# Performance work log

Measured on AMD Instinct MI355X. Metric: run time of the kernel, lower is better.

The kernel has to match this reference:

```python
import jax, jax.numpy as jnp
import numpy as np
from jax import lax

K = 5
WIN = (1, 1, K, K)
PAD = ((0, 0), (0, 0), (K // 2, K // 2), (K // 2, K // 2))
T_POOL = 0.9


def _conv(x, w, b, pad, dil=(1, 1), groups=1):
    y = lax.conv_general_dilated(x, w, (1, 1), pad, rhs_dilation=dil,
                                 dimension_numbers=('NCHW', 'OIHW', 'NCHW'),
                                 feature_group_count=groups)
    return y + b[None, :, None, None]


def _cbs(x, w, b):
    # Ultralytics Conv: 1x1 conv + folded-BN bias + SiLU
    return jax.nn.silu(_conv(x, w, b, ((0, 0), (0, 0))))


def _maxpool(x):
    return lax.reduce_window(x, -jnp.inf, lax.max, WIN, (1, 1, 1, 1), PAD)


def _sumpool(x):
    return lax.reduce_window(x, 0.0, lax.add, WIN, (1, 1, 1, 1), PAD)


def _tmaxavg(x):
    # TMaxAvgPool2d: blend of max pool and avg pool with weight T
    return T_POOL * _maxpool(x) + (1.0 - T_POOL) * (_sumpool(x) / (K * K))


def _rwpool(x):
    # RWPool2d: exponentially (response-) weighted pooling over the window
    c = lax.stop_gradient(jnp.max(x))  # constant shift, cancels exactly
    e = jnp.exp(x - c)
    return _sumpool(e * x) / (_sumpool(e) + 1e-6)


def setup_inputs():
    key = jax.random.key(0)
    ks = jax.random.split(key, 16)
    B, C1, H, W = 8, 512, 64, 64
    c_ = C1 // 2   # 256
    c4 = c_ * 4    # 1024
    C2 = 512
    f32 = jnp.float32

    def w(k, shape):
        return jax.random.normal(k, shape, f32) * 0.02

    return {
        'x': jax.random.normal(ks[0], (B, C1, H, W), f32),
        'w_sta': w(ks[1], (c_, C1, 1, 1)), 'b_sta': jnp.zeros((c_,), f32),
        'w_cv1': w(ks[2], (C2, c4, 1, 1)), 'b_cv1': jnp.zeros((C2,), f32),
        'w_cv2': w(ks[3], (C2, c4, 1, 1)), 'b_cv2': jnp.zeros((C2,), f32),
        'w_cvend': w(ks[4], (C2, c4, 1, 1)), 'b_cvend': jnp.zeros((C2,), f32),
        'w_dwh': w(ks[5], (c4, 1, 1, 3)), 'b_dwh': jnp.zeros((c4,), f32),
        'w_dwv': w(ks[6], (c4, 1, 3, 1)), 'b_dwv': jnp.zeros((c4,), f32),
        'w_ddwh': w(ks[7], (c4, 1, 1, 3)), 'b_ddwh': jnp.zeros((c4,), f32),
        'w_ddwv': w(ks[8], (c4, 1, 3, 1)), 'b_ddwv': jnp.zeros((c4,), f32),
        'w_c1': w(ks[9], (c4, c4, 1, 1)), 'b_c1': jnp.zeros((c4,), f32),
    }


def reference(x, w_sta, b_sta, w_cv1, b_cv1, w_cv2, b_cv2, w_cvend, b_cvend,
              w_dwh, b_dwh, w_dwv, b_dwv, w_ddwh, b_ddwh, w_ddwv, b_ddwv,
              w_c1, b_c1):
    x_aux = _cbs(x, w_sta, b_sta)                      # [B, c_, H, W]
    y1 = [x_aux]
    y2 = [x_aux]
    for _ in range(3):                                  # SPPF cascades
        y1.append(_tmaxavg(y1[-1]))
        y2.append(_rwpool(y2[-1]))
    y = jnp.concatenate([
        _cbs(jnp.concatenate(y1, 1), w_cv1, b_cv1),     # [B, c2, H, W]
        _cbs(jnp.concatenate(y2, 1), w_cv2, b_cv2),
    ], 1)                                               # [B, c_*4, H, W]
    C = y.shape[1]
    # LSKA: sequential depthwise convs -> 1x1 -> gating multiply
    a = _conv(y, w_dwh, b_dwh, ((0, 0), (1, 1)), groups=C)
    a = _conv(a, w_dwv, b_dwv, ((1, 1), (0, 0)), groups=C)
    a = _conv(a, w_ddwh, b_ddwh, ((0, 0), (2, 2)), dil=(1, 2), groups=C)
    a = _conv(a, w_ddwv, b_ddwv, ((2, 2), (0, 0)), dil=(2, 1), groups=C)
    a = _conv(a, w_c1, b_c1, ((0, 0), (0, 0)))
    return _cbs(y * a, w_cvend, b_cvend)                # [B, c2, H, W]
```

## Files before the change

### kernel.cpp

```cpp
#include <hip/hip_runtime.h>
#include <math.h>

typedef __attribute__((ext_vector_type(8))) short short8;
typedef __attribute__((ext_vector_type(16))) float floatx16;

__device__ __forceinline__ float silu_f(float v) { return v / (1.0f + expf(-v)); }
__device__ __forceinline__ float bf2f(unsigned short u) {
    unsigned int x = ((unsigned int)u) << 16;
    return __uint_as_float(x);
}
__device__ __forceinline__ unsigned short f2bf(float f) {
    unsigned int u = __float_as_uint(f);
    u += 0x7FFFu + ((u >> 16) & 1u);
    return (unsigned short)(u >> 16);
}

struct BSlots { const unsigned short* p[4]; };

#define APITCH 36
#define BPITCH 18

template <int EPI>
__global__ __launch_bounds__(256, 2)
void gemm_mfma(const unsigned short* __restrict__ Ahp,
               const unsigned short* __restrict__ Alp,
               const unsigned short* __restrict__ Ahp2,
               const unsigned short* __restrict__ Alp2, int ldK,
               BSlots bs, BSlots bs2, long bstride,
               const float* __restrict__ bias, const float* __restrict__ bias2,
               void* __restrict__ outv, int OC,
               const unsigned short* __restrict__ gate, int b0, int K)
{
    __shared__ __align__(16) unsigned short As[2][128 * APITCH];
    __shared__ __align__(16) unsigned int   Bsm[256 * BPITCH];

    const int t  = threadIdx.x;
    const int z  = blockIdx.z;
    const int m0 = blockIdx.y * 128;
    const int n0 = blockIdx.x * 256;

    int mA = m0;
    if (Ahp2 != nullptr && m0 >= 512) {
        Ahp = Ahp2; Alp = Alp2; bias = bias2; bs = bs2; mA = m0 - 512;
    }

    const int am = t >> 1, ahf = t & 1;
    const int bkg = t & 7, bn8 = t >> 3;

    const int w = t >> 6, lane = t & 63;
    const int wm = (w & 1) * 64, wn = (w >> 1) * 128;
    const int lm = lane & 31, q = lane >> 5;

    floatx16 acc[2][4];
#pragma unroll
    for (int i = 0; i < 2; ++i)
#pragma unroll
        for (int j = 0; j < 4; ++j)
#pragma unroll
            for (int r = 0; r < 16; ++r) acc[i][j][r] = 0.0f;

    const unsigned short* Aph = Ahp + (size_t)(mA + am) * ldK + ahf * 16;
    const unsigned short* Apl = Alp + (size_t)(mA + am) * ldK + ahf * 16;

    uint4 ah0, ah1, al0, al1, r0, r1, r2, r3;
    {
        ah0 = *(const uint4*)(Aph);
        ah1 = *(const uint4*)(Aph + 8);
        al0 = *(const uint4*)(Apl);
        al1 = *(const uint4*)(Apl + 8);
        const unsigned short* Bp = bs.p[0] + (size_t)z * bstride
                                 + (size_t)(bkg * 4) * 4096 + n0 + bn8 * 8;
        r0 = *(const uint4*)(Bp);
        r1 = *(const uint4*)(Bp + 4096);
        r2 = *(const uint4*)(Bp + 8192);
        r3 = *(const uint4*)(Bp + 12288);
    }

    for (int k0 = 0; k0 < K; k0 += 32) {
        __syncthreads();

        {
            unsigned short* Ad0 = &As[0][am * APITCH + ahf * 16];
            unsigned short* Ad1 = &As[1][am * APITCH + ahf * 16];
            ((uint2*)Ad0)[0] = *((const uint2*)&ah0);
            ((uint2*)Ad0)[1] = *((const uint2*)&ah0 + 1);
            ((uint2*)Ad0)[2] = *((const uint2*)&ah1);
            ((uint2*)Ad0)[3] = *((const uint2*)&ah1 + 1);
            ((uint2*)Ad1)[0] = *((const uint2*)&al0);
            ((uint2*)Ad1)[1] = *((const uint2*)&al0 + 1);
            ((uint2*)Ad1)[2] = *((const uint2*)&al1);
            ((uint2*)Ad1)[3] = *((const uint2*)&al1 + 1);
        }
        {
            const unsigned int* d0 = (const unsigned int*)&r0;
            const unsigned int* d1 = (const unsigned int*)&r1;
            const unsigned int* d2 = (const unsigned int*)&r2;
            const unsigned int* d3 = (const unsigned int*)&r3;
#pragma unroll
            for (int i = 0; i < 8; ++i) {
                unsigned int sel = (i & 1) ? 0x07060302u : 0x05040100u;
                uint2 pv;
                pv.x = __builtin_amdgcn_perm(d1[i >> 1], d0[i >> 1], sel);
                pv.y = __builtin_amdgcn_perm(d3[i >> 1], d2[i >> 1], sel);
                *(uint2*)&Bsm[(bn8 * 8 + i) * BPITCH + bkg * 2] = pv;
            }
        }
        __syncthreads();

        const int k1 = k0 + 32;
        if (k1 < K) {
            ah0 = *(const uint4*)(Aph + k1);
            ah1 = *(const uint4*)(Aph + k1 + 8);
            al0 = *(const uint4*)(Apl + k1);
            al1 = *(const uint4*)(Apl + k1 + 8);
            const unsigned short* Bp = bs.p[k1 >> 8] + (size_t)z * bstride
                                     + (size_t)((k1 & 255) + bkg * 4) * 4096
                                     + n0 + bn8 * 8;
            r0 = *(const uint4*)(Bp);
            r1 = *(const uint4*)(Bp + 4096);
            r2 = *(const uint4*)(Bp + 8192);
            r3 = *(const uint4*)(Bp + 12288);
        }

#pragma unroll
        for (int s = 0; s < 2; ++s) {
            union { short8 v; uint2 u[2]; } afh[2], afl[2], bfr[4];
#pragma unroll
            for (int i = 0; i < 2; ++i) {
                int rb = (wm + 32 * i + lm) * APITCH + s * 16 + q * 8;
                afh[i].u[0] = *(const uint2*)&As[0][rb];
                afh[i].u[1] = *(const uint2*)&As[0][rb + 4];
                afl[i].u[0] = *(const uint2*)&As[1][rb];
                afl[i].u[1] = *(const uint2*)&As[1][rb + 4];
            }
#pragma unroll
            for (int j = 0; j < 4; ++j) {
                int nb = (wn + 32 * j + lm) * BPITCH + s * 8 + q * 4;
                bfr[j].u[0] = *(const uint2*)&Bsm[nb];
                bfr[j].u[1] = *(const uint2*)&Bsm[nb + 2];
            }
#pragma unroll
            for (int i = 0; i < 2; ++i)
#pragma unroll
                for (int j = 0; j < 4; ++j) {
                    acc[i][j] = __builtin_amdgcn_mfma_f32_32x32x16_bf16(
                        afh[i].v, bfr[j].v, acc[i][j], 0, 0, 0);
                    acc[i][j] = __builtin_amdgcn_mfma_f32_32x32x16_bf16(
                        afl[i].v, bfr[j].v, acc[i][j], 0, 0, 0);
                }
        }
    }

#pragma unroll
    for (int i = 0; i < 2; ++i)
#pragma unroll
        for (int j = 0; j < 4; ++j)
#pragma unroll
            for (int r = 0; r < 16; ++r) {
                int row = wm + 32 * i + (r & 3) + 8 * (r >> 2) + 4 * q;
                int col = n0 + wn + 32 * j + lm;
                int mg  = m0 + row;
                size_t ob = ((size_t)z * OC + mg) * 4096 + col;
                float v = acc[i][j][r] + bias[mA + row];
                if (EPI == 0) {
                    ((unsigned short*)outv)[ob] = f2bf(silu_f(v));
                } else if (EPI == 1) {
                    float g = bf2f(gate[((size_t)(b0 + z) * 1024 + mg) * 4096 + col]);
                    ((unsigned short*)outv)[ob] = f2bf(v * g);
                } else {
                    ((float*)outv)[ob] = silu_f(v);
                }
            }
}

__global__ __launch_bounds__(512, 4)
void pool_casc_both(const unsigned short* __restrict__ in,
                    unsigned short* __restrict__ t1, unsigned short* __restrict__ t2,
                    unsigned short* __restrict__ t3, unsigned short* __restrict__ r1,
                    unsigned short* __restrict__ r2, unsigned short* __restrict__ r3)
{
    __shared__ float ha[4096], hb[4096];
    const size_t base = (size_t)blockIdx.x * 4096;
    const int t    = threadIdx.x;
    const int lane = t & 63;
    const int w    = t >> 6;

    const int il2 = (lane - 2) & 63, il1 = (lane - 1) & 63;
    const int ir1 = (lane + 1) & 63, ir2 = (lane + 2) & 63;
    const bool vl2 = lane >= 2, vl1 = lane >= 1;
    const bool vr1 = lane <= 62, vr2 = lane <= 61;

    float v[8];
#pragma unroll
    for (int k = 0; k < 8; ++k)
        v[k] = bf2f(in[base + (size_t)(w + 8 * k) * 64 + lane]);

#pragma unroll
    for (int s = 0; s < 3; ++s) {
        unsigned short* outp = (s == 0) ? t1 : (s == 1) ? t2 : t3;
#pragma unroll
        for (int k = 0; k < 8; ++k) {
            float c = v[k];
            float a2 = __shfl(c, il2, 64);
            float a1 = __shfl(c, il1, 64);
            float b1 = __shfl(c, ir1, 64);
            float b2 = __shfl(c, ir2, 64);
            float mx = -INFINITY, sm = 0.0f;
            mx = vl2 ? fmaxf(mx, a2) : mx;  sm = vl2 ? (sm + a2) : sm;
            mx = vl1 ? fmaxf(mx, a1) : mx;  sm = vl1 ? (sm + a1) : sm;
            mx = fmaxf(mx, c);              sm = sm + c;
            mx = vr1 ? fmaxf(mx, b1) : mx;  sm = vr1 ? (sm + b1) : sm;
            mx = vr2 ? fmaxf(mx, b2) : mx;  sm = vr2 ? (sm + b2) : sm;
            int r = w + 8 * k;
            ha[r * 64 + lane] = mx;
            hb[r * 64 + lane] = sm;
        }
        __syncthreads();
#pragma unroll
        for (int k = 0; k < 8; ++k) {
            int r = w + 8 * k;
            float mx = -INFINITY, sm = 0.0f;
#pragma unroll
            for (int dy = -2; dy <= 2; ++dy) {
                int rr = r + dy;
                if (0 <= rr && rr < 64) {
                    mx = fmaxf(mx, ha[rr * 64 + lane]);
                    sm += hb[rr * 64 + lane];
                }
            }
            float res = 0.9f * mx + 0.1f * (sm * (1.0f / 25.0f));
            v[k] = res;
            outp[base + (size_t)r * 64 + lane] = f2bf(res);
        }
        __syncthreads();
    }

#pragma unroll
    for (int k = 0; k < 8; ++k)
        v[k] = bf2f(in[base + (size_t)(w + 8 * k) * 64 + lane]);
#pragma unroll
    for (int s = 0; s < 3; ++s) {
        unsigned short* outp = (s == 0) ? r1 : (s == 1) ? r2 : r3;
#pragma unroll
        for (int k = 0; k < 8; ++k) {
            float c = v[k];
            float e = expf(c);
            float ea2 = __shfl(e, il2, 64), ca2 = __shfl(c, il2, 64);
            float ea1 = __shfl(e, il1, 64), ca1 = __shfl(c, il1, 64);
            float eb1 = __shfl(e, ir1, 64), cb1 = __shfl(c, ir1, 64);
            float eb2 = __shfl(e, ir2, 64), cb2 = __shfl(c, ir2, 64);
            float se = 0.0f, sx = 0.0f;
            se = vl2 ? (se + ea2) : se;  sx = vl2 ? (sx + ea2 * ca2) : sx;
            se = vl1 ? (se + ea1) : se;  sx = vl1 ? (sx + ea1 * ca1) : sx;
            se = se + e;                 sx = sx + e * c;
            se = vr1 ? (se + eb1) : se;  sx = vr1 ? (sx + eb1 * cb1) : sx;
            se = vr2 ? (se + eb2) : se;  sx = vr2 ? (sx + eb2 * cb2) : sx;
            int r = w + 8 * k;
            ha[r * 64 + lane] = sx;
            hb[r * 64 + lane] = se;
        }
        __syncthreads();
#pragma unroll
        for (int k = 0; k < 8; ++k) {
            int r = w + 8 * k;
            float se = 0.0f, sx = 0.0f;
#pragma unroll
            for (int dy = -2; dy <= 2; ++dy) {
                int rr = r + dy;
                if (0 <= rr && rr < 64) {
                    sx += ha[rr * 64 + lane];
                    se += hb[rr * 64 + lane];
                }
            }
            float res = sx / (se + 1e-6f);
            v[k] = res;
            outp[base + (size_t)r * 64 + lane] = f2bf(res);
        }
        __syncthreads();
    }
}

__global__ __launch_bounds__(256)
void lska_dw_quad(const unsigned short* __restrict__ Y2b, int b0,
                  const float* __restrict__ wh1, const float* __restrict__ bh1,
                  const float* __restrict__ wv1, const float* __restrict__ bv1,
                  const float* __restrict__ wh2, const float* __restrict__ bh2,
                  const float* __restrict__ wv2, const float* __restrict__ bv2,
                  unsigned short* __restrict__ outq)
{
    __shared__ float buf0[4096], buf1[4096];
    const int bi = blockIdx.x;
    const int zz = bi >> 10, c = bi & 1023;
    const unsigned short* src = Y2b + ((size_t)(b0 + zz) * 1024 + c) * 4096;
    unsigned short* dst = outq + (size_t)bi * 4096;
    const int t = threadIdx.x;
    for (int i = t; i < 4096; i += 256) buf0[i] = bf2f(src[i]);
    __syncthreads();
    {
        float w0 = wh1[c * 3], w1 = wh1[c * 3 + 1], w2 = wh1[c * 3 + 2], bb = bh1[c];
        for (int i = t; i < 4096; i += 256) {
            int x = i & 63;
            float a = fmaf(w1, buf0[i], bb);
            if (x >= 1)  a = fmaf(w0, buf0[i - 1], a);
            if (x <= 62) a = fmaf(w2, buf0[i + 1], a);
            buf1[i] = a;
        }
    }
    __syncthreads();
    {
        float w0 = wv1[c * 3], w1 = wv1[c * 3 + 1], w2 = wv1[c * 3 + 2], bb = bv1[c];
        for (int i = t; i < 4096; i += 256) {
            int y = i >> 6;
            float a = fmaf(w1, buf1[i], bb);
            if (y >= 1)  a = fmaf(w0, buf1[i - 64], a);
            if (y <= 62) a = fmaf(w2, buf1[i + 64], a);
            buf0[i] = a;
        }
    }
    __syncthreads();
    {
        float w0 = wh2[c * 3], w1 = wh2[c * 3 + 1], w2 = wh2[c * 3 + 2], bb = bh2[c];
        for (int i = t; i < 4096; i += 256) {
            int x = i & 63;
            float a = fmaf(w1, buf0[i], bb);
            if (x >= 2)  a = fmaf(w0, buf0[i - 2], a);
            if (x <= 61) a = fmaf(w2, buf0[i + 2], a);
            buf1[i] = a;
        }
    }
    __syncthreads();
    {
        float w0 = wv2[c * 3], w1 = wv2[c * 3 + 1], w2 = wv2[c * 3 + 2], bb = bv2[c];
        for (int i = t; i < 4096; i += 256) {
            int y = i >> 6;
            float a = fmaf(w1, buf1[i], bb);
            if (y >= 2)  a = fmaf(w0, buf1[i - 128], a);
            if (y <= 61) a = fmaf(w2, buf1[i + 128], a);
            dst[i] = f2bf(a);
        }
    }
}

__global__ void f2bf_vec(const float* __restrict__ in, unsigned short* __restrict__ out)
{
    size_t i = ((size_t)blockIdx.x * 256 + threadIdx.x) * 8;
    float4 v0 = *(const float4*)(in + i);
    float4 v1 = *(const float4*)(in + i + 4);
    uint2 o0, o1;
    o0.x = (unsigned)f2bf(v0.x) | ((unsigned)f2bf(v0.y) << 16);
    o0.y = (unsigned)f2bf(v0.z) | ((unsigned)f2bf(v0.w) << 16);
    o1.x = (unsigned)f2bf(v1.x) | ((unsigned)f2bf(v1.y) << 16);
    o1.y = (unsigned)f2bf(v1.z) | ((unsigned)f2bf(v1.w) << 16);
    *(uint2*)(out + i) = o0;
    *(uint2*)(out + i + 4) = o1;
}

__global__ void wsplit(const float* __restrict__ w, unsigned short* __restrict__ wh,
                       unsigned short* __restrict__ wl)
{
    int i = blockIdx.x * 256 + threadIdx.x;
    float v = w[i];
    unsigned short h = f2bf(v);
    wh[i] = h;
    wl[i] = f2bf(v - bf2f(h));
}

extern "C" void kernel_launch(void* const* d_in, const int* in_sizes, int n_in,
                              void* d_out, int out_size, void* d_ws, size_t ws_size,
                              hipStream_t stream)
{
    const float* x       = (const float*)d_in[0];
    const float* w_sta   = (const float*)d_in[1];
    const float* b_sta   = (const float*)d_in[2];
    const float* w_cv1   = (const float*)d_in[3];
    const float* b_cv1   = (const float*)d_in[4];
    const float* w_cv2   = (const float*)d_in[5];
    const float* b_cv2   = (const float*)d_in[6];
    const float* w_cvend = (const float*)d_in[7];
    const float* b_cvend = (const float*)d_in[8];
    const float* w_dwh   = (const float*)d_in[9];
    const float* b_dwh   = (const float*)d_in[10];
    const float* w_dwv   = (const float*)d_in[11];
    const float* b_dwv   = (const float*)d_in[12];
    const float* w_ddwh  = (const float*)d_in[13];
    const float* b_ddwh  = (const float*)d_in[14];
    const float* w_ddwv  = (const float*)d_in[15];
    const float* b_ddwv  = (const float*)d_in[16];
    const float* w_c1    = (const float*)d_in[17];
    const float* b_c1    = (const float*)d_in[18];
    float* outf = (float*)d_out;
    unsigned short* Y2b = (unsigned short*)d_out;

    unsigned short* WS   = (unsigned short*)d_ws;
    unsigned short* xaux = WS;
    unsigned short* t1   = WS + 8388608;
    unsigned short* t2   = WS + 16777216;
    unsigned short* t3   = WS + 25165824;
    unsigned short* r1   = WS + 33554432;
    unsigned short* r2   = WS + 41943040;
    unsigned short* r3   = WS + 50331648;
    unsigned short* WT   = WS + 58720256;
    unsigned short* xb   = t1;
    unsigned short* a4q  = WS;
    unsigned short* gq   = WS + 16777216;

    unsigned short* sta_h = WT,           * sta_l = WT + 131072;
    unsigned short* cv1_h = WT + 262144,  * cv1_l = WT + 786432;
    unsigned short* cv2_h = WT + 1310720, * cv2_l = WT + 1835008;
    unsigned short* c1_h  = WT + 2359296, * c1_l  = WT + 3407872;
    unsigned short* cve_h = WT + 4456448, * cve_l = WT + 4980736;

    dim3 blk(256);

    f2bf_vec<<<8192, blk, 0, stream>>>(x, xb);
    wsplit<<<512,  blk, 0, stream>>>(w_sta,   sta_h, sta_l);
    wsplit<<<2048, blk, 0, stream>>>(w_cv1,   cv1_h, cv1_l);
    wsplit<<<2048, blk, 0, stream>>>(w_cv2,   cv2_h, cv2_l);
    wsplit<<<4096, blk, 0, stream>>>(w_c1,    c1_h,  c1_l);
    wsplit<<<2048, blk, 0, stream>>>(w_cvend, cve_h, cve_l);

    {
        BSlots s; s.p[0] = xb; s.p[1] = xb + 1048576; s.p[2] = xb; s.p[3] = xb;
        gemm_mfma<0><<<dim3(16, 2, 8), blk, 0, stream>>>(
            sta_h, sta_l, nullptr, nullptr, 512, s, s, 2097152L,
            b_sta, nullptr, xaux, 256, nullptr, 0, 512);
    }

    pool_casc_both<<<2048, dim3(512), 0, stream>>>(xaux, t1, t2, t3, r1, r2, r3);

    {
        BSlots s1; s1.p[0] = xaux; s1.p[1] = t1; s1.p[2] = t2; s1.p[3] = t3;
        BSlots s2; s2.p[0] = xaux; s2.p[1] = r1; s2.p[2] = r2; s2.p[3] = r3;
        gemm_mfma<0><<<dim3(16, 8, 8), blk, 0, stream>>>(
            cv1_h, cv1_l, cv2_h, cv2_l, 1024, s1, s2, 1048576L,
            b_cv1, b_cv2, Y2b, 1024, nullptr, 0, 1024);
    }

    for (int qd = 0; qd < 2; ++qd) {
        const int b0 = 4 * qd;
        lska_dw_quad<<<4096, blk, 0, stream>>>(Y2b, b0,
                                               w_dwh, b_dwh, w_dwv, b_dwv,
                                               w_ddwh, b_ddwh, w_ddwv, b_ddwv, a4q);
        {
            BSlots s; s.p[0] = a4q; s.p[1] = a4q + 1048576;
            s.p[2] = a4q + 2097152; s.p[3] = a4q + 3145728;
            gemm_mfma<1><<<dim3(16, 8, 4), blk, 0, stream>>>(
                c1_h, c1_l, nullptr, nullptr, 1024, s, s, 4194304L,
                b_c1, nullptr, gq, 1024, Y2b, b0, 1024);
        }
        {
            BSlots s; s.p[0] = gq; s.p[1] = gq + 1048576;
            s.p[2] = gq + 2097152; s.p[3] = gq + 3145728;
            gemm_mfma<2><<<dim3(16, 4, 4), blk, 0, stream>>>(
                cve_h, cve_l, nullptr, nullptr, 1024, s, s, 4194304L,
                b_cvend, nullptr, outf + (size_t)b0 * 2097152, 512,
                nullptr, 0, 1024);
        }
    }
}
```

Measured before the change: 819.9 us.

## Use wave shuffles in LSKA depthwise chain and batch final GEMM across quads

The depthwise LSKA kernel now runs 512 threads, each keeping 8 rows in registers. Horizontal taps come from cross-lane shuffles, so two shared-memory passes and two barriers are dropped. The intermediate gated output for both batch quads is written to separate workspace regions so the final 1x1 GEMM runs as one launch over all 8 images. This relies on dead pooling buffers being reusable and raises register pressure in the depthwise kernel.

```diff
diff --git a/kernel.cpp b/kernel.cpp
--- a/kernel.cpp
+++ b/kernel.cpp
@@ -280,7 +280,7 @@
     }
 }
 
-__global__ __launch_bounds__(256)
+__global__ __launch_bounds__(512, 4)
 void lska_dw_quad(const unsigned short* __restrict__ Y2b, int b0,
                   const float* __restrict__ wh1, const float* __restrict__ bh1,
                   const float* __restrict__ wv1, const float* __restrict__ bv1,
@@ -288,56 +288,66 @@
                   const float* __restrict__ wv2, const float* __restrict__ bv2,
                   unsigned short* __restrict__ outq)
 {
-    __shared__ float buf0[4096], buf1[4096];
+    __shared__ float bufA[4096], bufB[4096];
     const int bi = blockIdx.x;
     const int zz = bi >> 10, c = bi & 1023;
     const unsigned short* src = Y2b + ((size_t)(b0 + zz) * 1024 + c) * 4096;
     unsigned short* dst = outq + (size_t)bi * 4096;
     const int t = threadIdx.x;
-    for (int i = t; i < 4096; i += 256) buf0[i] = bf2f(src[i]);
+    const int lane = t & 63, w = t >> 6;
+
+    const int il1 = (lane - 1) & 63, ir1 = (lane + 1) & 63;
+    const int il2 = (lane - 2) & 63, ir2 = (lane + 2) & 63;
+    const bool vl1 = lane >= 1, vr1 = lane <= 62;
+    const bool vl2 = lane >= 2, vr2 = lane <= 61;
+
+    const float h1w0 = wh1[c * 3], h1w1 = wh1[c * 3 + 1], h1w2 = wh1[c * 3 + 2], h1b = bh1[c];
+    const float v1w0 = wv1[c * 3], v1w1 = wv1[c * 3 + 1], v1w2 = wv1[c * 3 + 2], v1b = bv1[c];
+    const float h2w0 = wh2[c * 3], h2w1 = wh2[c * 3 + 1], h2w2 = wh2[c * 3 + 2], h2b = bh2[c];
+    const float v2w0 = wv2[c * 3], v2w1 = wv2[c * 3 + 1], v2w2 = wv2[c * 3 + 2], v2b = bv2[c];
+
+    float v[8];
+#pragma unroll
+    for (int k = 0; k < 8; ++k)
+        v[k] = bf2f(src[(size_t)(w + 8 * k) * 64 + lane]);
+
+#pragma unroll
+    for (int k = 0; k < 8; ++k) {
+        float cv = v[k];
+        float cl = __shfl(cv, il1, 64);
+        float cr = __shfl(cv, ir1, 64);
+        float a = fmaf(h1w1, cv, h1b);
+        a = vl1 ? fmaf(h1w0, cl, a) : a;
+        a = vr1 ? fmaf(h1w2, cr, a) : a;
+        bufA[(w + 8 * k) * 64 + lane] = a;
+    }
     __syncthreads();
-    {
-        float w0 = wh1[c * 3], w1 = wh1[c * 3 + 1], w2 = wh1[c * 3 + 2], bb = bh1[c];
-        for (int i = t; i < 4096; i += 256) {
-            int x = i & 63;
-            float a = fmaf(w1, buf0[i], bb);
-            if (x >= 1)  a = fmaf(w0, buf0[i - 1], a);
-            if (x <= 62) a = fmaf(w2, buf0[i + 1], a);
-            buf1[i] = a;
-        }
+#pragma unroll
+    for (int k = 0; k < 8; ++k) {
+        int r = w + 8 * k;
+        float a = fmaf(v1w1, bufA[r * 64 + lane], v1b);
+        if (r >= 1)  a = fmaf(v1w0, bufA[(r - 1) * 64 + lane], a);
+        if (r <= 62) a = fmaf(v1w2, bufA[(r + 1) * 64 + lane], a);
+        v[k] = a;
+    }
+#pragma unroll
+    for (int k = 0; k < 8; ++k) {
+        float cv = v[k];
+        float cl = __shfl(cv, il2, 64);
+        float cr = __shfl(cv, ir2, 64);
+        float a = fmaf(h2w1, cv, h2b);
+        a = vl2 ? fmaf(h2w0, cl, a) : a;
+        a = vr2 ? fmaf(h2w2, cr, a) : a;
+        bufB[(w + 8 * k) * 64 + lane] = a;
     }
     __syncthreads();
-    {
-        float w0 = wv1[c * 3], w1 = wv1[c * 3 + 1], w2 = wv1[c * 3 + 2], bb = bv1[c];
-        for (int i = t; i < 4096; i += 256) {
-            int y = i >> 6;
-            float a = fmaf(w1, buf1[i], bb);
-            if (y >= 1)  a = fmaf(w0, buf1[i - 64], a);
-            if (y <= 62) a = fmaf(w2, buf1[i + 64], a);
-            buf0[i] = a;
-        }
-    }
-    __syncthreads();
-    {
-        float w0 = wh2[c * 3], w1 = wh2[c * 3 + 1], w2 = wh2[c * 3 + 2], bb = bh2[c];
-        for (int i = t; i < 4096; i += 256) {
-            int x = i & 63;
-            float a = fmaf(w1, buf0[i], bb);
-            if (x >= 2)  a = fmaf(w0, buf0[i - 2], a);
-            if (x <= 61) a = fmaf(w2, buf0[i + 2], a);
-            buf1[i] = a;
-        }
-    }
-    __syncthreads();
-    {
-        float w0 = wv2[c * 3], w1 = wv2[c * 3 + 1], w2 = wv2[c * 3 + 2], bb = bv2[c];
-        for (int i = t; i < 4096; i += 256) {
-            int y = i >> 6;
-            float a = fmaf(w1, buf1[i], bb);
-            if (y >= 2)  a = fmaf(w0, buf1[i - 128], a);
-            if (y <= 61) a = fmaf(w2, buf1[i + 128], a);
-            dst[i] = f2bf(a);
-        }
+#pragma unroll
+    for (int k = 0; k < 8; ++k) {
+        int r = w + 8 * k;
+        float a = fmaf(v2w1, bufB[r * 64 + lane], v2b);
+        if (r >= 2)  a = fmaf(v2w0, bufB[(r - 2) * 64 + lane], a);
+        if (r <= 61) a = fmaf(v2w2, bufB[(r + 2) * 64 + lane], a);
+        dst[(size_t)r * 64 + lane] = f2bf(a);
     }
 }
 
@@ -402,7 +412,7 @@
     unsigned short* WT   = WS + 58720256;
     unsigned short* xb   = t1;
     unsigned short* a4q  = WS;
-    unsigned short* gq   = WS + 16777216;
+    unsigned short* gq8  = WS + 16777216;
 
     unsigned short* sta_h = WT,           * sta_l = WT + 131072;
     unsigned short* cv1_h = WT + 262144,  * cv1_l = WT + 786432;
@@ -438,7 +448,7 @@
 
     for (int qd = 0; qd < 2; ++qd) {
         const int b0 = 4 * qd;
-        lska_dw_quad<<<4096, blk, 0, stream>>>(Y2b, b0,
+        lska_dw_quad<<<4096, dim3(512), 0, stream>>>(Y2b, b0,
                                                w_dwh, b_dwh, w_dwv, b_dwv,
                                                w_ddwh, b_ddwh, w_ddwv, b_ddwv, a4q);
         {
@@ -446,15 +456,14 @@
             s.p[2] = a4q + 2097152; s.p[3] = a4q + 3145728;
             gemm_mfma<1><<<dim3(16, 8, 4), blk, 0, stream>>>(
                 c1_h, c1_l, nullptr, nullptr, 1024, s, s, 4194304L,
-                b_c1, nullptr, gq, 1024, Y2b, b0, 1024);
-        }
-        {
-            BSlots s; s.p[0] = gq; s.p[1] = gq + 1048576;
-            s.p[2] = gq + 2097152; s.p[3] = gq + 3145728;
-            gemm_mfma<2><<<dim3(16, 4, 4), blk, 0, stream>>>(
-                cve_h, cve_l, nullptr, nullptr, 1024, s, s, 4194304L,
-                b_cvend, nullptr, outf + (size_t)b0 * 2097152, 512,
-                nullptr, 0, 1024);
-        }
-    }
-}
+                b_c1, nullptr, gq8 + (size_t)qd * 16777216, 1024, Y2b, b0, 1024);
+        }
+    }
+    {
+        BSlots s; s.p[0] = gq8; s.p[1] = gq8 + 1048576;
+        s.p[2] = gq8 + 2097152; s.p[3] = gq8 + 3145728;
+        gemm_mfma<2><<<dim3(16, 4, 8), blk, 0, stream>>>(
+            cve_h, cve_l, nullptr, nullptr, 1024, s, s, 4194304L,
+            b_cvend, nullptr, outf, 512, nullptr, 0, 1024);
+    }
+}
```

New measurement: 761.6 us. -7.1%, faster.
